# Kernel tuning notes

Measured on AMD Instinct MI355X. Metric: run time of the kernel, lower is better.

## Reference

```python
import jax, jax.numpy as jnp
import numpy as np

BN_EPS = 1e-5
OUT_H, OUT_W = 32, 32  # crop_size / output_stride = 512/16


def setup_inputs() -> dict:
    key = jax.random.key(0)
    k1, k2, k3, k4 = jax.random.split(key, 4)
    x = jax.random.normal(k1, (16, 2048, 32, 32), dtype=jnp.float32)
    # conv1x1 weight, bias-free: [dim_out, dim_in]
    W = jax.random.normal(k2, (256, 2048), dtype=jnp.float32) * (1.0 / np.sqrt(2048.0))
    gamma = jax.random.normal(k3, (256,), dtype=jnp.float32) * 0.1 + 1.0
    beta = jax.random.normal(k4, (256,), dtype=jnp.float32) * 0.1
    return {"x": x, "W": W, "gamma": gamma, "beta": beta}


def reference(x, W, gamma, beta):
    # 1x1 conv, no bias: channel contraction
    y = jnp.einsum("nchw,oc->nohw", x, W)  # [N, dim_out, H, W]
    # BatchNorm2d in training mode: batch statistics over (N, H, W), biased var
    mean = jnp.mean(y, axis=(0, 2, 3), keepdims=True)
    var = jnp.mean(jnp.square(y - mean), axis=(0, 2, 3), keepdims=True)
    g = gamma.reshape(1, -1, 1, 1)
    b = beta.reshape(1, -1, 1, 1)
    y = g * (y - mean) * jax.lax.rsqrt(var + BN_EPS) + b
    # global average pool to 1x1
    pooled = jnp.mean(y, axis=(2, 3), keepdims=True)  # [N, dim_out, 1, 1]
    # adaptive avg pool from 1x1 to (OUT_H, OUT_W) is a pure broadcast
    out = jnp.broadcast_to(pooled, pooled.shape[:2] + (OUT_H, OUT_W))
    return out
```

## Files before the change

kernel.cpp:

```cpp
#include <hip/hip_runtime.h>
#include <hip/hip_bf16.h>
#include <stdint.h>

#define NB    16
#define CIN   2048
#define OUTC  256
#define HW    1024
#define BJ    64
#define BK    64
#define NJT   (HW / BJ)
#define NKS   2
#define KSL   (CIN / BK / NKS)
#define NPART (NKS * NB * NJT)

typedef __attribute__((ext_vector_type(8))) short bf16x8;
typedef __attribute__((ext_vector_type(4))) float f32x4;
typedef __attribute__((ext_vector_type(4))) unsigned int u32x4;

__device__ __forceinline__ unsigned int f2bf(float f) {
    union { float f; unsigned int u; } a; a.f = f;
    return (a.u + 0x7FFFu + ((a.u >> 16) & 1u)) >> 16;
}

__device__ __forceinline__ void block_sync_lds() {
    asm volatile("s_waitcnt lgkmcnt(0)" ::: "memory");
    __builtin_amdgcn_s_barrier();
    asm volatile("" ::: "memory");
}

__global__ void wprep_kernel(const float* __restrict__ W, unsigned short* __restrict__ Afrag) {
    int g  = blockIdx.x * blockDim.x + threadIdx.x;
    int o  = g >> 8;
    int kc = g & 255;
    const float4* p = reinterpret_cast<const float4*>(W + o * CIN + kc * 8);
    float4 v0 = p[0], v1 = p[1];
    u32x4 pk;
    pk.x = f2bf(v0.x) | (f2bf(v0.y) << 16);
    pk.y = f2bf(v0.z) | (f2bf(v0.w) << 16);
    pk.z = f2bf(v1.x) | (f2bf(v1.y) << 16);
    pk.w = f2bf(v1.z) | (f2bf(v1.w) << 16);
    int ks32 = kc >> 2, g8 = kc & 3;
    int lane = g8 * 16 + (o & 15), ot = o >> 4;
    *reinterpret_cast<u32x4*>(Afrag + (((size_t)ks32 * 16 + ot) * 64 + lane) * 8) = pk;
}

__global__ __launch_bounds__(512, 4) void gemm_stats_kernel(
    const float* __restrict__ x,
    const unsigned short* __restrict__ Afrag,
    float* __restrict__ s1_part,
    float* __restrict__ s2_part)
{
    __shared__ __align__(16) unsigned short B0[4096], B1[4096];

    const int tid    = threadIdx.x;
    const int lane   = tid & 63;
    const int wave   = tid >> 6;
    const int blk    = blockIdx.x;
    const int kslice = blk >> 8;
    const int n      = (blk >> 4) & 15;
    const int jt     = blk & 15;
    const int j0     = jt * BJ;

    const float* xn = x + (size_t)n * CIN * HW + (size_t)kslice * (CIN / NKS) * HW;

    const int bj = tid & 63;
    const int kh = tid >> 6;
    const float* Bgp = xn + (size_t)(kh * 8) * HW + j0 + bj;
    const int offB = (kh >> 2) * 2048 + (bj >> 4) * 512 + (kh & 3) * 128 + (bj & 15) * 8;

    const int rbase = lane * 8;

    const unsigned short* Ab = Afrag + (size_t)kslice * (KSL * 2 * 16 * 64 * 8) + lane * 8;

#define LDA(ks, R) { _Pragma("unroll") \
    for (int h = 0; h < 2; ++h) _Pragma("unroll") for (int t = 0; t < 2; ++t) \
        R[h * 2 + t] = *(const u32x4*)(Ab + ((((ks) * 2 + h) * 16 + 2 * wave + t) * 64) * 8); }
#define LDB(ks, F) { const float* p = Bgp + (size_t)(ks) * BK * HW; \
    _Pragma("unroll") for (int i = 0; i < 8; ++i) F[i] = p[(size_t)i * HW]; }
#define WRITEB(Bb, F) { u32x4 pk; \
    pk.x = f2bf(F[0]) | (f2bf(F[1]) << 16); pk.y = f2bf(F[2]) | (f2bf(F[3]) << 16); \
    pk.z = f2bf(F[4]) | (f2bf(F[5]) << 16); pk.w = f2bf(F[6]) | (f2bf(F[7]) << 16); \
    *(u32x4*)&Bb[offB] = pk; }
#define COMPUTE(Bb, R) { _Pragma("unroll") \
    for (int h = 0; h < 2; ++h) { \
        bf16x8 af0 = *(const bf16x8*)&R[h * 2 + 0]; \
        bf16x8 af1 = *(const bf16x8*)&R[h * 2 + 1]; \
        _Pragma("unroll") \
        for (int ni = 0; ni < 4; ++ni) { \
            bf16x8 bf = *(const bf16x8*)&Bb[h * 2048 + ni * 512 + rbase]; \
            acc[0][ni] = __builtin_amdgcn_mfma_f32_16x16x32_bf16(af0, bf, acc[0][ni], 0, 0, 0); \
            acc[1][ni] = __builtin_amdgcn_mfma_f32_16x16x32_bf16(af1, bf, acc[1][ni], 0, 0, 0); \
    } } }

    f32x4 acc[2][4] = {};
    u32x4 Ra[4];
    float Bs0[8], Bs1[8];

    LDB(0, Bs0); LDB(1, Bs1);
    LDA(0, Ra);
    WRITEB(B0, Bs0);
    LDB(2, Bs0);
    block_sync_lds();

    #pragma unroll 1
    for (int ks = 0; ks < KSL; ks += 2) {
        COMPUTE(B0, Ra);
        LDA(ks + 1, Ra);
        WRITEB(B1, Bs1);
        {
            int kb = (ks + 3 < KSL) ? ks + 3 : KSL - 1;
            LDB(kb, Bs1);
        }
        block_sync_lds();
        COMPUTE(B1, Ra);
        {
            int ka = (ks + 2 < KSL) ? ks + 2 : KSL - 1;
            LDA(ka, Ra);
        }
        if (ks + 2 < KSL) {
            WRITEB(B0, Bs0);
            int kb = (ks + 4 < KSL) ? ks + 4 : KSL - 1;
            LDB(kb, Bs0);
            block_sync_lds();
        }
    }

    float rs[2][4], rq[2][4];
    #pragma unroll
    for (int mi = 0; mi < 2; ++mi) {
        #pragma unroll
        for (int r = 0; r < 4; ++r) {
            float s = 0.f, q = 0.f;
            #pragma unroll
            for (int ni = 0; ni < 4; ++ni) {
                float v = acc[mi][ni][r];
                s += v; q += v * v;
            }
            rs[mi][r] = s; rq[mi][r] = q;
        }
    }
    #pragma unroll
    for (int m = 1; m < 16; m <<= 1) {
        #pragma unroll
        for (int mi = 0; mi < 2; ++mi) {
            #pragma unroll
            for (int r = 0; r < 4; ++r) {
                rs[mi][r] += __shfl_xor(rs[mi][r], m, 64);
                rq[mi][r] += __shfl_xor(rq[mi][r], m, 64);
            }
        }
    }
    if ((lane & 15) == 0) {
        const int gK = lane >> 4;
        #pragma unroll
        for (int mi = 0; mi < 2; ++mi) {
            #pragma unroll
            for (int r = 0; r < 4; ++r) {
                int o = wave * 32 + mi * 16 + gK * 4 + r;
                s1_part[(size_t)blk * OUTC + o] = rs[mi][r];
                s2_part[(size_t)blk * OUTC + o] = rq[mi][r];
            }
        }
    }
#undef LDA
#undef LDB
#undef WRITEB
#undef COMPUTE
}

__global__ __launch_bounds__(256) void finalize_bcast_kernel(
    const float* __restrict__ s1_part,
    const float* __restrict__ s2_part,
    const float* __restrict__ gamma,
    const float* __restrict__ beta,
    float* __restrict__ out)
{
    const int tid   = threadIdx.x;
    const int slice = tid & 15;
    const int o_l   = tid >> 4;
    const int n0    = blockIdx.x >> 4;
    const int o     = (blockIdx.x & 15) * 16 + o_l;

    float S1 = 0.f, S2 = 0.f;
    #pragma unroll
    for (int q = 0; q < 32; ++q) {
        int p = slice * 32 + q;
        S1 += s1_part[p * OUTC + o];
        S2 += s2_part[p * OUTC + o];
    }
    float s1n = s1_part[((0 * NB + n0) * NJT + slice) * OUTC + o]
              + s1_part[((1 * NB + n0) * NJT + slice) * OUTC + o];
    #pragma unroll
    for (int m = 1; m < 16; m <<= 1) {
        S1  += __shfl_xor(S1, m, 64);
        S2  += __shfl_xor(S2, m, 64);
        s1n += __shfl_xor(s1n, m, 64);
    }
    float mean = S1 * (1.f / 16384.f);
    float var  = S2 * (1.f / 16384.f) - mean * mean;
    float inv  = rsqrtf(var + 1e-5f);
    float v = gamma[o] * (s1n * (1.f / 1024.f) - mean) * inv + beta[o];

    float4 vv = make_float4(v, v, v, v);
    float4* dst = reinterpret_cast<float4*>(out + ((size_t)(n0 * OUTC + o)) * HW);
    #pragma unroll
    for (int it = 0; it < 16; ++it)
        dst[it * 16 + slice] = vv;
}

extern "C" void kernel_launch(void* const* d_in, const int* in_sizes, int n_in,
                              void* d_out, int out_size, void* d_ws, size_t ws_size,
                              hipStream_t stream) {
    const float* x     = (const float*)d_in[0];
    const float* W     = (const float*)d_in[1];
    const float* gamma = (const float*)d_in[2];
    const float* beta  = (const float*)d_in[3];
    float* out = (float*)d_out;

    char* ws = (char*)d_ws;
    unsigned short* Afrag = (unsigned short*)ws;
    float* s1_part = (float*)(ws + (1 << 20));
    float* s2_part = (float*)(ws + (1 << 20) + (512 << 10));

    hipLaunchKernelGGL(wprep_kernel, dim3(256), dim3(256), 0, stream, W, Afrag);
    hipLaunchKernelGGL(gemm_stats_kernel, dim3(NPART), dim3(512), 0, stream,
                       x, Afrag, s1_part, s2_part);
    hipLaunchKernelGGL(finalize_bcast_kernel, dim3(NB * (OUTC / 16)), dim3(256), 0, stream,
                       s1_part, s2_part, gamma, beta, out);
}
```

Measured before the change: 49.16 us.

## Halve GEMM block to 4 waves, each computing 64 output channels

Shrinks the GEMM+stats block from 8 to 4 waves. Each wave now covers 64 output channels (4x4 MFMA tiles) instead of 32, and each thread loads 16 x values per k-step instead of 8. A fragments are double-buffered in registers (Aa0/Aa1) to prefetch further ahead. The goal is more MFMA work per LDS B-fragment read and fewer barriers per unit of work, at the cost of more registers per thread and lower occupancy (launch bounds 256,2).

```diff
diff --git a/kernel.cpp b/kernel.cpp
--- a/kernel.cpp
+++ b/kernel.cpp
@@ -44,7 +44,7 @@
     *reinterpret_cast<u32x4*>(Afrag + (((size_t)ks32 * 16 + ot) * 64 + lane) * 8) = pk;
 }
 
-__global__ __launch_bounds__(512, 4) void gemm_stats_kernel(
+__global__ __launch_bounds__(256, 2) void gemm_stats_kernel(
     const float* __restrict__ x,
     const unsigned short* __restrict__ Afrag,
     float* __restrict__ s1_part,
@@ -64,70 +64,70 @@
     const float* xn = x + (size_t)n * CIN * HW + (size_t)kslice * (CIN / NKS) * HW;
 
     const int bj = tid & 63;
-    const int kh = tid >> 6;
-    const float* Bgp = xn + (size_t)(kh * 8) * HW + j0 + bj;
-    const int offB = (kh >> 2) * 2048 + (bj >> 4) * 512 + (kh & 3) * 128 + (bj & 15) * 8;
+    const int kq = tid >> 6;
+    const float* Bgp = xn + (size_t)(kq * 8) * HW + j0 + bj;
+    const int offB = (bj >> 4) * 512 + kq * 128 + (bj & 15) * 8;
 
     const int rbase = lane * 8;
-
-    const unsigned short* Ab = Afrag + (size_t)kslice * (KSL * 2 * 16 * 64 * 8) + lane * 8;
-
+    const unsigned short* Ab = Afrag
+        + (size_t)kslice * (KSL * 2 * 16 * 64 * 8) + (size_t)lane * 8;
+
+#define CLMP(v) (((v) < KSL) ? (v) : KSL - 1)
 #define LDA(ks, R) { _Pragma("unroll") \
-    for (int h = 0; h < 2; ++h) _Pragma("unroll") for (int t = 0; t < 2; ++t) \
-        R[h * 2 + t] = *(const u32x4*)(Ab + ((((ks) * 2 + h) * 16 + 2 * wave + t) * 64) * 8); }
+    for (int h = 0; h < 2; ++h) _Pragma("unroll") for (int mi = 0; mi < 4; ++mi) \
+        R[h * 4 + mi] = *(const u32x4*)(Ab + ((((ks) * 2 + h) * 16 + wave * 4 + mi) * 64) * 8); }
 #define LDB(ks, F) { const float* p = Bgp + (size_t)(ks) * BK * HW; \
-    _Pragma("unroll") for (int i = 0; i < 8; ++i) F[i] = p[(size_t)i * HW]; }
+    _Pragma("unroll") for (int i = 0; i < 8; ++i) F[i] = p[(size_t)i * HW]; \
+    _Pragma("unroll") for (int i = 0; i < 8; ++i) F[8 + i] = p[(size_t)(32 + i) * HW]; }
 #define WRITEB(Bb, F) { u32x4 pk; \
     pk.x = f2bf(F[0]) | (f2bf(F[1]) << 16); pk.y = f2bf(F[2]) | (f2bf(F[3]) << 16); \
     pk.z = f2bf(F[4]) | (f2bf(F[5]) << 16); pk.w = f2bf(F[6]) | (f2bf(F[7]) << 16); \
-    *(u32x4*)&Bb[offB] = pk; }
+    *(u32x4*)&Bb[offB] = pk; \
+    pk.x = f2bf(F[8]) | (f2bf(F[9]) << 16);   pk.y = f2bf(F[10]) | (f2bf(F[11]) << 16); \
+    pk.z = f2bf(F[12]) | (f2bf(F[13]) << 16); pk.w = f2bf(F[14]) | (f2bf(F[15]) << 16); \
+    *(u32x4*)&Bb[offB + 2048] = pk; }
 #define COMPUTE(Bb, R) { _Pragma("unroll") \
-    for (int h = 0; h < 2; ++h) { \
-        bf16x8 af0 = *(const bf16x8*)&R[h * 2 + 0]; \
-        bf16x8 af1 = *(const bf16x8*)&R[h * 2 + 1]; \
+    for (int h = 0; h < 2; ++h) _Pragma("unroll") for (int ni = 0; ni < 4; ++ni) { \
+        bf16x8 bf = *(const bf16x8*)&Bb[h * 2048 + ni * 512 + rbase]; \
         _Pragma("unroll") \
-        for (int ni = 0; ni < 4; ++ni) { \
-            bf16x8 bf = *(const bf16x8*)&Bb[h * 2048 + ni * 512 + rbase]; \
-            acc[0][ni] = __builtin_amdgcn_mfma_f32_16x16x32_bf16(af0, bf, acc[0][ni], 0, 0, 0); \
-            acc[1][ni] = __builtin_amdgcn_mfma_f32_16x16x32_bf16(af1, bf, acc[1][ni], 0, 0, 0); \
+        for (int mi = 0; mi < 4; ++mi) { \
+            bf16x8 af = *(const bf16x8*)&R[h * 4 + mi]; \
+            acc[mi][ni] = __builtin_amdgcn_mfma_f32_16x16x32_bf16(af, bf, acc[mi][ni], 0, 0, 0); \
     } } }
 
-    f32x4 acc[2][4] = {};
-    u32x4 Ra[4];
-    float Bs0[8], Bs1[8];
-
-    LDB(0, Bs0); LDB(1, Bs1);
-    LDA(0, Ra);
-    WRITEB(B0, Bs0);
-    LDB(2, Bs0);
+    f32x4 acc[4][4] = {};
+    u32x4 Aa0[8], Aa1[8];
+    float BsA[16], BsB[16];
+
+    LDA(0, Aa0); LDB(0, BsA);
+    LDA(1, Aa1); LDB(1, BsB);
+    WRITEB(B0, BsA);
+    LDB(2, BsA);
     block_sync_lds();
 
     #pragma unroll 1
     for (int ks = 0; ks < KSL; ks += 2) {
-        COMPUTE(B0, Ra);
-        LDA(ks + 1, Ra);
-        WRITEB(B1, Bs1);
+        COMPUTE(B0, Aa0);
         {
-            int kb = (ks + 3 < KSL) ? ks + 3 : KSL - 1;
-            LDB(kb, Bs1);
-        }
-        block_sync_lds();
-        COMPUTE(B1, Ra);
+            LDA(CLMP(ks + 2), Aa0);
+            WRITEB(B1, BsB);
+            LDB(CLMP(ks + 3), BsB);
+            block_sync_lds();
+        }
+        COMPUTE(B1, Aa1);
         {
-            int ka = (ks + 2 < KSL) ? ks + 2 : KSL - 1;
-            LDA(ka, Ra);
+            LDA(CLMP(ks + 3), Aa1);
         }
         if (ks + 2 < KSL) {
-            WRITEB(B0, Bs0);
-            int kb = (ks + 4 < KSL) ? ks + 4 : KSL - 1;
-            LDB(kb, Bs0);
+            WRITEB(B0, BsA);
+            LDB(CLMP(ks + 4), BsA);
             block_sync_lds();
         }
     }
 
-    float rs[2][4], rq[2][4];
-    #pragma unroll
-    for (int mi = 0; mi < 2; ++mi) {
+    float rs[4][4], rq[4][4];
+    #pragma unroll
+    for (int mi = 0; mi < 4; ++mi)
         #pragma unroll
         for (int r = 0; r < 4; ++r) {
             float s = 0.f, q = 0.f;
@@ -138,30 +138,27 @@
             }
             rs[mi][r] = s; rq[mi][r] = q;
         }
-    }
-    #pragma unroll
-    for (int m = 1; m < 16; m <<= 1) {
+    #pragma unroll
+    for (int m = 1; m < 16; m <<= 1)
         #pragma unroll
-        for (int mi = 0; mi < 2; ++mi) {
+        for (int mi = 0; mi < 4; ++mi)
             #pragma unroll
             for (int r = 0; r < 4; ++r) {
                 rs[mi][r] += __shfl_xor(rs[mi][r], m, 64);
                 rq[mi][r] += __shfl_xor(rq[mi][r], m, 64);
             }
-        }
-    }
     if ((lane & 15) == 0) {
         const int gK = lane >> 4;
         #pragma unroll
-        for (int mi = 0; mi < 2; ++mi) {
+        for (int mi = 0; mi < 4; ++mi)
             #pragma unroll
             for (int r = 0; r < 4; ++r) {
-                int o = wave * 32 + mi * 16 + gK * 4 + r;
+                int o = wave * 64 + mi * 16 + gK * 4 + r;
                 s1_part[(size_t)blk * OUTC + o] = rs[mi][r];
                 s2_part[(size_t)blk * OUTC + o] = rq[mi][r];
             }
-        }
-    }
+    }
+#undef CLMP
 #undef LDA
 #undef LDB
 #undef WRITEB
@@ -223,7 +220,7 @@
     float* s2_part = (float*)(ws + (1 << 20) + (512 << 10));
 
     hipLaunchKernelGGL(wprep_kernel, dim3(256), dim3(256), 0, stream, W, Afrag);
-    hipLaunchKernelGGL(gemm_stats_kernel, dim3(NPART), dim3(512), 0, stream,
+    hipLaunchKernelGGL(gemm_stats_kernel, dim3(NPART), dim3(256), 0, stream,
                        x, Afrag, s1_part, s2_part);
     hipLaunchKernelGGL(finalize_bcast_kernel, dim3(NB * (OUTC / 16)), dim3(256), 0, stream,
                        s1_part, s2_part, gamma, beta, out);
```

Result: no change. 49.09 us (-0.1%).
